# Kernel tuning notes

Hardware: AMD Instinct MI355X
Metric: run time of the kernel (lower is better)

The kernel has to match this reference:

```python
import jax, jax.numpy as jnp
import numpy as np

B, T, C, H = 4, 2048, 1024, 16
D = C // H  # head_dim = 64


def setup_inputs() -> dict:
    key = jax.random.key(0)
    k1, k2, k3, k4 = jax.random.split(key, 4)
    x = jax.random.normal(k1, (B, T, C), dtype=jnp.float32)
    # realistic padding: each sequence has length in [T//2, T]
    lengths = jax.random.randint(k4, (B,), T // 2, T + 1)
    padding_mask = jnp.arange(T)[None, :] < lengths[:, None]  # True = keep
    # weights stored [in, out] (equivalent to torch Linear weight transposed)
    w_qkv = jax.random.normal(k2, (C, 3 * C), dtype=jnp.float32) * (C ** -0.5)
    w_out = jax.random.normal(k3, (C, C), dtype=jnp.float32) * (C ** -0.5)
    b_out = jnp.zeros((C,), dtype=jnp.float32)
    return {"x": x, "padding_mask": padding_mask, "w_qkv": w_qkv, "w_out": w_out, "b_out": b_out}


def reference(x, padding_mask, w_qkv, w_out, b_out):
    scale = D ** -0.5
    qkv = x @ w_qkv  # [B,T,3C]
    q, k, v = jnp.split(qkv, 3, axis=-1)

    def split_heads(t):
        return t.reshape(B, T, H, D).transpose(0, 2, 1, 3)  # [B,H,T,D]

    q, k, v = split_heads(q), split_heads(k), split_heads(v)
    attn = jnp.einsum("bhqd,bhkd->bhqk", q, k) * scale  # [B,H,T,T]
    mask = padding_mask[:, None, None, :]  # [B,1,1,T]
    attn = jnp.where(mask, attn, jnp.finfo(attn.dtype).min)
    attn = jax.nn.softmax(attn, axis=-1)
    # dropout is identity in eval mode
    out = jnp.einsum("bhqk,bhkd->bhqd", attn, v)  # [B,H,T,D]
    out = out.transpose(0, 2, 1, 3).reshape(B, T, C)
    return out @ w_out + b_out
```

## Files before the change

kernel.cpp:

```cpp
#include <hip/hip_runtime.h>
#include <hip/hip_bf16.h>

#define Bb 4
#define Tt 2048
#define Cc 1024
#define Hh 16

typedef unsigned short u16;
typedef __attribute__((ext_vector_type(8))) __bf16 bf16x8;
typedef __attribute__((ext_vector_type(4))) float  f32x4;

__device__ __forceinline__ u16 f2bf_hw(float f) {
    __bf16 h = (__bf16)f;
    return *(u16*)&h;
}

__device__ __forceinline__ unsigned cvt_pk_bf16(float a, float b) {
    unsigned r;
    asm("v_cvt_pk_bf16_f32 %0, %1, %2" : "=v"(r) : "v"(a), "v"(b));
    return r;
}

__device__ __forceinline__ float fexp2(float x) {
#if __has_builtin(__builtin_amdgcn_exp2f)
    return __builtin_amdgcn_exp2f(x);
#else
    return __expf(x * 0.6931471805599453f);
#endif
}

__device__ __forceinline__ void gld_lds16(const void* g, void* l) {
    __builtin_amdgcn_global_load_lds(
        (__attribute__((address_space(1))) void*)(g),
        (__attribute__((address_space(3))) void*)(l),
        16, 0, 0);
}

__device__ __forceinline__ f32x4 mfma16(bf16x8 a, bf16x8 b, f32x4 c) {
    return __builtin_amdgcn_mfma_f32_16x16x32_bf16(a, b, c, 0, 0, 0);
}

__device__ void castT_body(const float* __restrict__ in, u16* __restrict__ out,
                           int K, int N, int scaleN, float sv,
                           int bx, int by, float Ls[64][65]) {
    const int n0 = bx * 64, k0 = by * 64;
    const int t = threadIdx.x;
    #pragma unroll
    for (int s = 0; s < 4; ++s) {
        int idx = t + 256 * s;
        int r   = idx >> 4;
        int c4  = (idx & 15) * 4;
        float4 v = *(const float4*)&in[(size_t)(k0 + r) * N + n0 + c4];
        Ls[r][c4 + 0] = v.x; Ls[r][c4 + 1] = v.y;
        Ls[r][c4 + 2] = v.z; Ls[r][c4 + 3] = v.w;
    }
    __syncthreads();
    #pragma unroll
    for (int s = 0; s < 2; ++s) {
        int idx = t + 256 * s;
        int n   = idx >> 3;
        int kc  = (idx & 7) * 8;
        const float sc = (n0 + n < scaleN) ? sv : 1.0f;
        alignas(16) u16 tmp[8];
        #pragma unroll
        for (int i = 0; i < 8; ++i) tmp[i] = f2bf_hw(Ls[kc + i][n] * sc);
        *(uint4*)&out[(size_t)(n0 + n) * K + k0 + kc] = *(const uint4*)tmp;
    }
}

__global__ void prep_cast(const float* __restrict__ x, u16* __restrict__ xb,
                          const float* __restrict__ w_qkv, u16* __restrict__ wqkvT,
                          const float* __restrict__ w_out, u16* __restrict__ woutT,
                          float c2) {
    __shared__ float Ls[64][65];
    const int id = blockIdx.x;
    if (id < 8192) {
        const int i = id * 256 + threadIdx.x;
        float4 v = ((const float4*)x)[i];
        uint2 o;
        o.x = cvt_pk_bf16(v.x, v.y);
        o.y = cvt_pk_bf16(v.z, v.w);
        ((uint2*)xb)[i] = o;
    } else if (id < 8192 + 768) {
        const int r = id - 8192;
        castT_body(w_qkv, wqkvT, Cc, 3 * Cc, Cc, c2, r % 48, r / 48, Ls);
    } else {
        const int r = id - 8960;
        castT_body(w_out, woutT, Cc, Cc, 0, 1.0f, r % 16, r / 16, Ls);
    }
}

__global__ __launch_bounds__(256, 3) void gemm_bt_bf16(
    const u16* __restrict__ A, const u16* __restrict__ Bt,
    const float* __restrict__ bias,
    u16* __restrict__ outB, float* __restrict__ outF,
    int M, int N, int K)
{
    __shared__ u16 As[128 * 64];
    __shared__ u16 Bs[128 * 64];
    const int t = threadIdx.x;
    const int w = t >> 6, lane = t & 63;
    const int quad = lane >> 4, l16 = lane & 15;
    const int wm = w >> 1, wn = w & 1;
    const int m0 = blockIdx.y * 128, n0 = blockIdx.x * 128;

    const int l8r   = lane >> 3;
    const int g_log = (lane & 7) ^ l8r;
    const u16* sAp[4]; const u16* sBp[4];
    #pragma unroll
    for (int u = 0; u < 4; ++u) {
        const int gi = w * 4 + u;
        sAp[u] = A  + (size_t)(m0 + gi * 8 + l8r) * K + g_log * 8;
        sBp[u] = Bt + (size_t)(n0 + gi * 8 + l8r) * K + g_log * 8;
    }
    const int dst0 = w * 2048 + lane * 8;

    int aoff[4][2], boff[4][2];
    #pragma unroll
    for (int i = 0; i < 4; ++i) {
        const int rA = 64 * wm + 16 * i + l16;
        const int rB = 64 * wn + 16 * i + l16;
        #pragma unroll
        for (int kk = 0; kk < 2; ++kk) {
            aoff[i][kk] = rA * 64 + (((4 * kk + quad) ^ (rA & 7)) * 8);
            boff[i][kk] = rB * 64 + (((4 * kk + quad) ^ (rB & 7)) * 8);
        }
    }

    f32x4 acc[4][4] = {};

    for (int k0 = 0; k0 < K; k0 += 64) {
        __syncthreads();
        #pragma unroll
        for (int u = 0; u < 4; ++u) {
            gld_lds16(sAp[u] + k0, (void*)(As + dst0 + u * 512));
            gld_lds16(sBp[u] + k0, (void*)(Bs + dst0 + u * 512));
        }
        asm volatile("s_waitcnt vmcnt(0)" ::: "memory");
        __syncthreads();

        #pragma unroll
        for (int kk = 0; kk < 2; ++kk) {
            bf16x8 af[4], bfr[4];
            #pragma unroll
            for (int i = 0; i < 4; ++i) af[i]  = *(const bf16x8*)&As[aoff[i][kk]];
            #pragma unroll
            for (int j = 0; j < 4; ++j) bfr[j] = *(const bf16x8*)&Bs[boff[j][kk]];
            #pragma unroll
            for (int i = 0; i < 4; ++i)
                #pragma unroll
                for (int j = 0; j < 4; ++j)
                    acc[i][j] = mfma16(af[i], bfr[j], acc[i][j]);
        }
    }

    const int rbase = m0 + 64 * wm + quad * 4;
    const int cbase = n0 + 64 * wn + l16;
    if (outF) {
        float bv[4];
        #pragma unroll
        for (int j = 0; j < 4; ++j) bv[j] = bias[cbase + 16 * j];
        #pragma unroll
        for (int i = 0; i < 4; ++i)
            #pragma unroll
            for (int r = 0; r < 4; ++r) {
                size_t ro = (size_t)(rbase + 16 * i + r) * N;
                #pragma unroll
                for (int j = 0; j < 4; ++j)
                    outF[ro + cbase + 16 * j] = acc[i][j][r] + bv[j];
            }
    } else {
        #pragma unroll
        for (int i = 0; i < 4; ++i)
            #pragma unroll
            for (int r = 0; r < 4; ++r) {
                size_t ro = (size_t)(rbase + 16 * i + r) * N;
                #pragma unroll
                for (int j = 0; j < 4; ++j)
                    outB[ro + cbase + 16 * j] = f2bf_hw(acc[i][j][r]);
            }
    }
}

__global__ __launch_bounds__(256, 3) void gemm_qkv_bt(
    const u16* __restrict__ A, const u16* __restrict__ Bt,
    u16* __restrict__ outQ, u16* __restrict__ kx, u16* __restrict__ vx)
{
    const int K = Cc;
    __shared__ u16 As[128 * 64];
    __shared__ u16 Bs[128 * 64];
    const int t = threadIdx.x;
    const int w = t >> 6, lane = t & 63;
    const int quad = lane >> 4, l16 = lane & 15;
    const int wm = w >> 1, wn = w & 1;
    const int m0 = blockIdx.y * 128, n0 = blockIdx.x * 128;

    const int l8r   = lane >> 3;
    const int g_log = (lane & 7) ^ l8r;
    const u16* sAp[4]; const u16* sBp[4];
    #pragma unroll
    for (int u = 0; u < 4; ++u) {
        const int gi = w * 4 + u;
        sAp[u] = A  + (size_t)(m0 + gi * 8 + l8r) * K + g_log * 8;
        sBp[u] = Bt + (size_t)(n0 + gi * 8 + l8r) * K + g_log * 8;
    }
    const int dst0 = w * 2048 + lane * 8;

    int aoff[4][2], boff[4][2];
    #pragma unroll
    for (int i = 0; i < 4; ++i) {
        const int rA = 64 * wm + 16 * i + l16;
        const int rB = 64 * wn + 16 * i + l16;
        #pragma unroll
        for (int kk = 0; kk < 2; ++kk) {
            aoff[i][kk] = rA * 64 + (((4 * kk + quad) ^ (rA & 7)) * 8);
            boff[i][kk] = rB * 64 + (((4 * kk + quad) ^ (rB & 7)) * 8);
        }
    }

    f32x4 acc[4][4] = {};

    for (int k0 = 0; k0 < K; k0 += 64) {
        __syncthreads();
        #pragma unroll
        for (int u = 0; u < 4; ++u) {
            gld_lds16(sAp[u] + k0, (void*)(As + dst0 + u * 512));
            gld_lds16(sBp[u] + k0, (void*)(Bs + dst0 + u * 512));
        }
        asm volatile("s_waitcnt vmcnt(0)" ::: "memory");
        __syncthreads();

        #pragma unroll
        for (int kk = 0; kk < 2; ++kk) {
            bf16x8 af[4], bfr[4];
            #pragma unroll
            for (int i = 0; i < 4; ++i) af[i]  = *(const bf16x8*)&As[aoff[i][kk]];
            #pragma unroll
            for (int j = 0; j < 4; ++j) bfr[j] = *(const bf16x8*)&Bs[boff[j][kk]];
            #pragma unroll
            for (int i = 0; i < 4; ++i)
                #pragma unroll
                for (int j = 0; j < 4; ++j)
                    acc[i][j] = mfma16(af[i], bfr[j], acc[i][j]);
        }
    }

    const int rbase = m0 + 64 * wm + quad * 4;
    const int cbase = n0 + 64 * wn + l16;
    const int region = n0 >> 10;

    if (region == 0) {
        #pragma unroll
        for (int i = 0; i < 4; ++i)
            #pragma unroll
            for (int r = 0; r < 4; ++r) {
                size_t ro = (size_t)(rbase + 16 * i + r) * Cc;
                #pragma unroll
                for (int j = 0; j < 4; ++j)
                    outQ[ro + cbase + 16 * j] = f2bf_hw(acc[i][j][r]);
            }
    } else if (region == 1) {
        int colK[4];
        #pragma unroll
        for (int j = 0; j < 4; ++j) {
            const int c = (cbase - 1024) + 16 * j;
            const int h = c >> 6, d = c & 63;
            colK[j] = h * 131072 + (d >> 5) * 512 + ((d >> 3) & 3) * 128 + (d & 7);
        }
        #pragma unroll
        for (int i = 0; i < 4; ++i)
            #pragma unroll
            for (int r = 0; r < 4; ++r) {
                const int row = rbase + 16 * i + r;
                const int b = row >> 11, key = row & 2047;
                const int ch = key >> 6, keyr = key & 63;
                const int rowK = b * 2097152 + ch * 4096 + (keyr >> 4) * 1024 + (keyr & 15) * 8;
                #pragma unroll
                for (int j = 0; j < 4; ++j)
                    kx[rowK + colK[j]] = f2bf_hw(acc[i][j][r]);
            }
    } else {
        int colV[4];
        #pragma unroll
        for (int j = 0; j < 4; ++j) {
            const int c = (cbase - 2048) + 16 * j;
            const int h = c >> 6, d = c & 63;
            colV[j] = h * 131072 + (d >> 4) * 1024 + (d & 15) * 8;
        }
        #pragma unroll
        for (int i = 0; i < 4; ++i)
            #pragma unroll
            for (int r = 0; r < 4; ++r) {
                const int row = rbase + 16 * i + r;
                const int b = row >> 11, key = row & 2047;
                const int ch = key >> 6, keyr = key & 63;
                const int rowV = b * 2097152 + ch * 4096 + (keyr >> 5) * 512
                               + ((keyr >> 3) & 3) * 128 + (keyr & 7);
                #pragma unroll
                for (int j = 0; j < 4; ++j)
                    vx[rowV + colV[j]] = f2bf_hw(acc[i][j][r]);
            }
    }
}

__global__ __launch_bounds__(256, 2) void attn_mfma4(
    const u16* __restrict__ qb, const u16* __restrict__ kx, const u16* __restrict__ vx,
    const int* __restrict__ mask, u16* __restrict__ outO)
{
    __shared__ u16 KVs[8192];
    __shared__ u16 Pss[4][4][16 * 68];

    const int t = threadIdx.x;
    const int w = t >> 6, lane = t & 63;
    const int quad = lane >> 4, l16 = lane & 15;
    const int bh = blockIdx.x, qblk = blockIdx.y, b = bh >> 4, h = bh & 15;

    int sum = 0;
    {
        const int4* mp = (const int4*)(mask + b * Tt) + lane * 8;
        #pragma unroll
        for (int i = 0; i < 8; ++i) { int4 m4 = mp[i]; sum += m4.x + m4.y + m4.z + m4.w; }
        #pragma unroll
        for (int off = 1; off < 64; off <<= 1) sum += __shfl_xor(sum, off);
    }
    const int L = sum;

    const int q0 = qblk * 256 + w * 64;
    bf16x8 qf[4][2];
    #pragma unroll
    for (int qq = 0; qq < 4; ++qq) {
        const u16* qp = qb + (size_t)(b * Tt + q0 + 16 * qq + l16) * Cc + h * 64 + quad * 8;
        qf[qq][0] = *(const bf16x8*)(qp);
        qf[qq][1] = *(const bf16x8*)(qp + 32);
    }

    f32x4 oacc[4][4] = {};
    f32x4 lacc[4]    = {};
    const __bf16 onebf = (__bf16)1.0f;
    const bf16x8 ones  = {onebf, onebf, onebf, onebf, onebf, onebf, onebf, onebf};

    const int nfull = L >> 6;
    const int nch   = (L + 63) >> 6;
    const size_t cb0 = (size_t)bh * 32 * 4096;

    {
        uint4 k0a = *(const uint4*)&kx[cb0 + t * 8];
        uint4 k0b = *(const uint4*)&kx[cb0 + 2048 + t * 8];
        uint4 v0a = *(const uint4*)&vx[cb0 + t * 8];
        uint4 v0b = *(const uint4*)&vx[cb0 + 2048 + t * 8];
        *(uint4*)&KVs[t * 8]        = k0a;
        *(uint4*)&KVs[2048 + t * 8] = k0b;
        *(uint4*)&KVs[4096 + t * 8] = v0a;
        *(uint4*)&KVs[6144 + t * 8] = v0b;
    }
    __syncthreads();

    for (int ch = 0; ch < nch; ++ch) {
        const int cc = (ch + 1 < nch) ? ch + 1 : ch;
        const size_t nb = cb0 + (size_t)cc * 4096;
        uint4 nk0 = *(const uint4*)&kx[nb + t * 8];
        uint4 nk1 = *(const uint4*)&kx[nb + 2048 + t * 8];
        uint4 nv0 = *(const uint4*)&vx[nb + t * 8];
        uint4 nv1 = *(const uint4*)&vx[nb + 2048 + t * 8];

        const u16* Kb = KVs;
        const u16* Vb = KVs + 4096;

        bf16x8 kf[4][2];
        #pragma unroll
        for (int jt = 0; jt < 4; ++jt)
            #pragma unroll
            for (int ks = 0; ks < 2; ++ks)
                kf[jt][ks] = *(const bf16x8*)&Kb[(jt * 2 + ks) * 512 + lane * 8];

        bf16x8 vf[4][2];
        #pragma unroll
        for (int dt = 0; dt < 4; ++dt)
            #pragma unroll
            for (int ks = 0; ks < 2; ++ks)
                vf[dt][ks] = *(const bf16x8*)&Vb[(dt * 2 + ks) * 512 + lane * 8];

        #pragma unroll
        for (int qq = 0; qq < 4; ++qq) {
            u16* Pw = Pss[w][qq];
            f32x4 st[4];
            __builtin_amdgcn_s_setprio(1);
            #pragma unroll
            for (int jt = 0; jt < 4; ++jt) {
                f32x4 z = {0.f, 0.f, 0.f, 0.f};
                z = mfma16(kf[jt][0], qf[qq][0], z);
                st[jt] = mfma16(kf[jt][1], qf[qq][1], z);
            }
            __builtin_amdgcn_s_setprio(0);
            uint2 pk[4];
            if (ch < nfull) {
                #pragma unroll
                for (int jt = 0; jt < 4; ++jt) {
                    pk[jt].x = cvt_pk_bf16(fexp2(st[jt][0]), fexp2(st[jt][1]));
                    pk[jt].y = cvt_pk_bf16(fexp2(st[jt][2]), fexp2(st[jt][3]));
                }
            } else {
                const int kc = ch * 64;
                #pragma unroll
                for (int jt = 0; jt < 4; ++jt) {
                    const int kb = kc + 16 * jt + quad * 4;
                    float e[4];
                    #pragma unroll
                    for (int r = 0; r < 4; ++r)
                        e[r] = (kb + r < L) ? fexp2(st[jt][r]) : 0.f;
                    pk[jt].x = cvt_pk_bf16(e[0], e[1]);
                    pk[jt].y = cvt_pk_bf16(e[2], e[3]);
                }
            }
            #pragma unroll
            for (int jt = 0; jt < 4; ++jt)
                *(uint2*)&Pw[l16 * 68 + 16 * jt + quad * 4] = pk[jt];

            __builtin_amdgcn_s_setprio(1);
            #pragma unroll
            for (int ks = 0; ks < 2; ++ks) {
                const u16* pr = &Pw[l16 * 68 + 32 * ks + quad * 8];
                uint2 pa = *(const uint2*)pr;
                uint2 pb = *(const uint2*)(pr + 4);
                uint4 comb = {pa.x, pa.y, pb.x, pb.y};
                bf16x8 pf = *(const bf16x8*)&comb;
                #pragma unroll
                for (int dt = 0; dt < 4; ++dt)
                    oacc[qq][dt] = mfma16(pf, vf[dt][ks], oacc[qq][dt]);
                lacc[qq] = mfma16(pf, ones, lacc[qq]);
            }
            __builtin_amdgcn_s_setprio(0);
        }

        __syncthreads();
        *(uint4*)&KVs[t * 8]        = nk0;
        *(uint4*)&KVs[2048 + t * 8] = nk1;
        *(uint4*)&KVs[4096 + t * 8] = nv0;
        *(uint4*)&KVs[6144 + t * 8] = nv1;
        __syncthreads();
    }

    #pragma unroll
    for (int qq = 0; qq < 4; ++qq)
        #pragma unroll
        for (int r = 0; r < 4; ++r) {
            const float inv = 1.f / lacc[qq][r];
            const size_t ro = (size_t)(b * Tt + q0 + 16 * qq + quad * 4 + r) * Cc + h * 64 + l16;
            #pragma unroll
            for (int dt = 0; dt < 4; ++dt)
                outO[ro + 16 * dt] = f2bf_hw(oacc[qq][dt][r] * inv);
        }
}

extern "C" void kernel_launch(void* const* d_in, const int* in_sizes, int n_in,
                              void* d_out, int out_size, void* d_ws, size_t ws_size,
                              hipStream_t stream) {
    const float* x     = (const float*)d_in[0];
    const int*   mask  = (const int*)  d_in[1];
    const float* w_qkv = (const float*)d_in[2];
    const float* w_out = (const float*)d_in[3];
    const float* b_out = (const float*)d_in[4];
    float*       outp  = (float*)d_out;

    const int M = Bb * Tt;
    char* ws = (char*)d_ws;
    u16* xb     = (u16*)(ws);
    u16* wqkvT  = (u16*)(ws + (16u << 20));
    u16* woutT  = (u16*)(ws + (22u << 20));
    u16* qbuf   = (u16*)(ws + (24u << 20));
    u16* kx     = (u16*)(ws + (40u << 20));
    u16* vx     = (u16*)(ws + (56u << 20));
    u16* attnO  = (u16*)(ws);

    const float c2 = 0.18033688011112042f;

    prep_cast<<<9216, 256, 0, stream>>>(x, xb, w_qkv, wqkvT, w_out, woutT, c2);

    gemm_qkv_bt<<<dim3(3 * Cc / 128, M / 128), 256, 0, stream>>>(
        xb, wqkvT, qbuf, kx, vx);

    attn_mfma4<<<dim3(Bb * Hh, Tt / 256), 256, 0, stream>>>(qbuf, kx, vx, mask, attnO);

    gemm_bt_bf16<<<dim3(Cc / 128, M / 128), 256, 0, stream>>>(
        attnO, woutT, b_out, nullptr, outp, M, Cc, Cc);
}
```

Baseline: 239.5 us.

## Rewrite attention kernel with 32x32 MFMA, register-resident P, and async LDS double buffering

The attention kernel moves from 16x16x32 to 32x32x16 bf16 MFMA tiles with 8 waves of 32 queries each. The probability tile now stays in registers, rearranged with v_permlane32_swap, which removes the LDS round-trip for P. The row sum is accumulated in scalar registers and combined through LDS, replacing the extra ones-MFMA. K/V chunks are double-buffered with global_load_lds, and the QKV GEMM epilogue rewrites the K/V storage layout to match the new operand order. The risks are lower occupancy (512 threads, one block per CU), K/V fragments now reloaded from LDS for each tile, and a correctness dependence on the new swizzle layouts.

```diff
diff --git a/kernel.cpp b/kernel.cpp
--- a/kernel.cpp
+++ b/kernel.cpp
@@ -9,6 +9,7 @@
 typedef unsigned short u16;
 typedef __attribute__((ext_vector_type(8))) __bf16 bf16x8;
 typedef __attribute__((ext_vector_type(4))) float  f32x4;
+typedef __attribute__((ext_vector_type(16))) float f32x16;
 
 __device__ __forceinline__ u16 f2bf_hw(float f) {
     __bf16 h = (__bf16)f;
@@ -19,6 +20,10 @@
     unsigned r;
     asm("v_cvt_pk_bf16_f32 %0, %1, %2" : "=v"(r) : "v"(a), "v"(b));
     return r;
+}
+
+__device__ __forceinline__ void plswap(unsigned &d, unsigned &s) {
+    asm("v_permlane32_swap_b32 %0, %1" : "+v"(d), "+v"(s));
 }
 
 __device__ __forceinline__ float fexp2(float x) {
@@ -38,6 +43,9 @@
 
 __device__ __forceinline__ f32x4 mfma16(bf16x8 a, bf16x8 b, f32x4 c) {
     return __builtin_amdgcn_mfma_f32_16x16x32_bf16(a, b, c, 0, 0, 0);
+}
+__device__ __forceinline__ f32x16 mfma32(bf16x8 a, bf16x8 b, f32x16 c) {
+    return __builtin_amdgcn_mfma_f32_32x32x16_bf16(a, b, c, 0, 0, 0);
 }
 
 __device__ void castT_body(const float* __restrict__ in, u16* __restrict__ out,
@@ -265,16 +273,17 @@
         for (int j = 0; j < 4; ++j) {
             const int c = (cbase - 1024) + 16 * j;
             const int h = c >> 6, d = c & 63;
-            colK[j] = h * 131072 + (d >> 5) * 512 + ((d >> 3) & 3) * 128 + (d & 7);
+            colK[j] = h * 131072 + (d >> 4) * 512 + ((d >> 3) & 1) * 256 + (d & 7);
         }
         #pragma unroll
         for (int i = 0; i < 4; ++i)
             #pragma unroll
             for (int r = 0; r < 4; ++r) {
                 const int row = rbase + 16 * i + r;
-                const int b = row >> 11, key = row & 2047;
-                const int ch = key >> 6, keyr = key & 63;
-                const int rowK = b * 2097152 + ch * 4096 + (keyr >> 4) * 1024 + (keyr & 15) * 8;
+                const int b = row >> 11, keyb = row & 2047;
+                const int ch = keyb >> 6, keyr = keyb & 63;
+                const int rowK = b * 2097152 + ch * 4096
+                               + (keyr >> 5) * 2048 + (keyr & 31) * 8;
                 #pragma unroll
                 for (int j = 0; j < 4; ++j)
                     kx[rowK + colK[j]] = f2bf_hw(acc[i][j][r]);
@@ -285,17 +294,18 @@
         for (int j = 0; j < 4; ++j) {
             const int c = (cbase - 2048) + 16 * j;
             const int h = c >> 6, d = c & 63;
-            colV[j] = h * 131072 + (d >> 4) * 1024 + (d & 15) * 8;
+            colV[j] = h * 131072 + (d >> 5) * 512 + (d & 31) * 8;
         }
         #pragma unroll
         for (int i = 0; i < 4; ++i)
             #pragma unroll
             for (int r = 0; r < 4; ++r) {
                 const int row = rbase + 16 * i + r;
-                const int b = row >> 11, key = row & 2047;
-                const int ch = key >> 6, keyr = key & 63;
-                const int rowV = b * 2097152 + ch * 4096 + (keyr >> 5) * 512
-                               + ((keyr >> 3) & 3) * 128 + (keyr & 7);
+                const int b = row >> 11, keyb = row & 2047;
+                const int ch = keyb >> 6, keyr = keyb & 63;
+                const int rowV = b * 2097152 + ch * 4096
+                               + (keyr >> 5) * 2048 + ((keyr >> 4) & 1) * 1024
+                               + ((keyr >> 3) & 1) * 256 + (keyr & 7);
                 #pragma unroll
                 for (int j = 0; j < 4; ++j)
                     vx[rowV + colV[j]] = f2bf_hw(acc[i][j][r]);
@@ -303,17 +313,17 @@
     }
 }
 
-__global__ __launch_bounds__(256, 2) void attn_mfma4(
+__global__ __launch_bounds__(512, 1) void attn_mfma32(
     const u16* __restrict__ qb, const u16* __restrict__ kx, const u16* __restrict__ vx,
     const int* __restrict__ mask, u16* __restrict__ outO)
 {
-    __shared__ u16 KVs[8192];
-    __shared__ u16 Pss[4][4][16 * 68];
+    __shared__ u16 KVs[2][8192];
+    __shared__ float LS[8][64];
 
     const int t = threadIdx.x;
     const int w = t >> 6, lane = t & 63;
-    const int quad = lane >> 4, l16 = lane & 15;
-    const int bh = blockIdx.x, qblk = blockIdx.y, b = bh >> 4, h = bh & 15;
+    const int c32 = lane & 31, h5 = lane >> 5;
+    const int bh = blockIdx.x, qblk = blockIdx.y, b = bh >> 4, hh = bh & 15;
 
     int sum = 0;
     {
@@ -325,131 +335,101 @@
     }
     const int L = sum;
 
-    const int q0 = qblk * 256 + w * 64;
-    bf16x8 qf[4][2];
-    #pragma unroll
-    for (int qq = 0; qq < 4; ++qq) {
-        const u16* qp = qb + (size_t)(b * Tt + q0 + 16 * qq + l16) * Cc + h * 64 + quad * 8;
-        qf[qq][0] = *(const bf16x8*)(qp);
-        qf[qq][1] = *(const bf16x8*)(qp + 32);
-    }
-
-    f32x4 oacc[4][4] = {};
-    f32x4 lacc[4]    = {};
-    const __bf16 onebf = (__bf16)1.0f;
-    const bf16x8 ones  = {onebf, onebf, onebf, onebf, onebf, onebf, onebf, onebf};
+    const int q0w = qblk * 256 + w * 32;
+    bf16x8 qf[4];
+    {
+        const u16* qp = qb + (size_t)(b * Tt + q0w + c32) * Cc + hh * 64 + h5 * 8;
+        #pragma unroll
+        for (int ds = 0; ds < 4; ++ds)
+            qf[ds] = *(const bf16x8*)(qp + 16 * ds);
+    }
+
+    f32x16 oacc[2] = {};
+    float ls = 0.f;
 
     const int nfull = L >> 6;
     const int nch   = (L + 63) >> 6;
-    const size_t cb0 = (size_t)bh * 32 * 4096;
-
-    {
-        uint4 k0a = *(const uint4*)&kx[cb0 + t * 8];
-        uint4 k0b = *(const uint4*)&kx[cb0 + 2048 + t * 8];
-        uint4 v0a = *(const uint4*)&vx[cb0 + t * 8];
-        uint4 v0b = *(const uint4*)&vx[cb0 + 2048 + t * 8];
-        *(uint4*)&KVs[t * 8]        = k0a;
-        *(uint4*)&KVs[2048 + t * 8] = k0b;
-        *(uint4*)&KVs[4096 + t * 8] = v0a;
-        *(uint4*)&KVs[6144 + t * 8] = v0b;
-    }
+    const size_t cb0 = (size_t)bh * 131072;
+
+    gld_lds16(kx + cb0 + t * 8, &KVs[0][t * 8]);
+    gld_lds16(vx + cb0 + t * 8, &KVs[0][4096 + t * 8]);
     __syncthreads();
 
     for (int ch = 0; ch < nch; ++ch) {
+        const int p = ch & 1;
         const int cc = (ch + 1 < nch) ? ch + 1 : ch;
         const size_t nb = cb0 + (size_t)cc * 4096;
-        uint4 nk0 = *(const uint4*)&kx[nb + t * 8];
-        uint4 nk1 = *(const uint4*)&kx[nb + 2048 + t * 8];
-        uint4 nv0 = *(const uint4*)&vx[nb + t * 8];
-        uint4 nv1 = *(const uint4*)&vx[nb + 2048 + t * 8];
-
-        const u16* Kb = KVs;
-        const u16* Vb = KVs + 4096;
-
-        bf16x8 kf[4][2];
-        #pragma unroll
-        for (int jt = 0; jt < 4; ++jt)
-            #pragma unroll
-            for (int ks = 0; ks < 2; ++ks)
-                kf[jt][ks] = *(const bf16x8*)&Kb[(jt * 2 + ks) * 512 + lane * 8];
-
-        bf16x8 vf[4][2];
-        #pragma unroll
-        for (int dt = 0; dt < 4; ++dt)
-            #pragma unroll
-            for (int ks = 0; ks < 2; ++ks)
-                vf[dt][ks] = *(const bf16x8*)&Vb[(dt * 2 + ks) * 512 + lane * 8];
-
-        #pragma unroll
-        for (int qq = 0; qq < 4; ++qq) {
-            u16* Pw = Pss[w][qq];
-            f32x4 st[4];
+        gld_lds16(kx + nb + t * 8, &KVs[p ^ 1][t * 8]);
+        gld_lds16(vx + nb + t * 8, &KVs[p ^ 1][4096 + t * 8]);
+
+        const u16* Kb = KVs[p];
+        const u16* Vb = KVs[p] + 4096;
+
+        #pragma unroll
+        for (int jt = 0; jt < 2; ++jt) {
+            f32x16 st = {};
             __builtin_amdgcn_s_setprio(1);
             #pragma unroll
-            for (int jt = 0; jt < 4; ++jt) {
-                f32x4 z = {0.f, 0.f, 0.f, 0.f};
-                z = mfma16(kf[jt][0], qf[qq][0], z);
-                st[jt] = mfma16(kf[jt][1], qf[qq][1], z);
+            for (int ds = 0; ds < 4; ++ds) {
+                bf16x8 kf = *(const bf16x8*)&Kb[jt * 2048 + ds * 512 + lane * 8];
+                st = mfma32(kf, qf[ds], st);
             }
             __builtin_amdgcn_s_setprio(0);
-            uint2 pk[4];
+
+            float e[16];
             if (ch < nfull) {
                 #pragma unroll
-                for (int jt = 0; jt < 4; ++jt) {
-                    pk[jt].x = cvt_pk_bf16(fexp2(st[jt][0]), fexp2(st[jt][1]));
-                    pk[jt].y = cvt_pk_bf16(fexp2(st[jt][2]), fexp2(st[jt][3]));
+                for (int r = 0; r < 16; ++r) e[r] = fexp2(st[r]);
+            } else {
+                const int kcb = ch * 64 + 32 * jt + 4 * h5;
+                #pragma unroll
+                for (int r = 0; r < 16; ++r) {
+                    const int key = kcb + (r & 3) + 8 * (r >> 2);
+                    e[r] = (key < L) ? fexp2(st[r]) : 0.f;
                 }
-            } else {
-                const int kc = ch * 64;
-                #pragma unroll
-                for (int jt = 0; jt < 4; ++jt) {
-                    const int kb = kc + 16 * jt + quad * 4;
-                    float e[4];
-                    #pragma unroll
-                    for (int r = 0; r < 4; ++r)
-                        e[r] = (kb + r < L) ? fexp2(st[jt][r]) : 0.f;
-                    pk[jt].x = cvt_pk_bf16(e[0], e[1]);
-                    pk[jt].y = cvt_pk_bf16(e[2], e[3]);
+            }
+            #pragma unroll
+            for (int r = 0; r < 16; ++r) ls += e[r];
+
+            unsigned W[4][2];
+            #pragma unroll
+            for (int s = 0; s < 4; ++s)
+                #pragma unroll
+                for (int i = 0; i < 2; ++i)
+                    W[s][i] = cvt_pk_bf16(e[4 * s + 2 * i], e[4 * s + 2 * i + 1]);
+
+            #pragma unroll
+            for (int ks = 0; ks < 2; ++ks) {
+                unsigned w0 = W[2 * ks][0], w2 = W[2 * ks + 1][0];
+                unsigned w1 = W[2 * ks][1], w3 = W[2 * ks + 1][1];
+                plswap(w0, w2);
+                plswap(w1, w3);
+                uint4 pfw = {w0, w1, w2, w3};
+                bf16x8 pf = *(const bf16x8*)&pfw;
+                __builtin_amdgcn_s_setprio(1);
+                #pragma unroll
+                for (int dt = 0; dt < 2; ++dt) {
+                    bf16x8 vf = *(const bf16x8*)&Vb[jt * 2048 + ks * 1024 + dt * 512 + lane * 8];
+                    oacc[dt] = mfma32(pf, vf, oacc[dt]);
                 }
-            }
-            #pragma unroll
-            for (int jt = 0; jt < 4; ++jt)
-                *(uint2*)&Pw[l16 * 68 + 16 * jt + quad * 4] = pk[jt];
-
-            __builtin_amdgcn_s_setprio(1);
-            #pragma unroll
-            for (int ks = 0; ks < 2; ++ks) {
-                const u16* pr = &Pw[l16 * 68 + 32 * ks + quad * 8];
-                uint2 pa = *(const uint2*)pr;
-                uint2 pb = *(const uint2*)(pr + 4);
-                uint4 comb = {pa.x, pa.y, pb.x, pb.y};
-                bf16x8 pf = *(const bf16x8*)&comb;
-                #pragma unroll
-                for (int dt = 0; dt < 4; ++dt)
-                    oacc[qq][dt] = mfma16(pf, vf[dt][ks], oacc[qq][dt]);
-                lacc[qq] = mfma16(pf, ones, lacc[qq]);
-            }
-            __builtin_amdgcn_s_setprio(0);
+                __builtin_amdgcn_s_setprio(0);
+            }
         }
 
         __syncthreads();
-        *(uint4*)&KVs[t * 8]        = nk0;
-        *(uint4*)&KVs[2048 + t * 8] = nk1;
-        *(uint4*)&KVs[4096 + t * 8] = nv0;
-        *(uint4*)&KVs[6144 + t * 8] = nv1;
-        __syncthreads();
-    }
-
-    #pragma unroll
-    for (int qq = 0; qq < 4; ++qq)
-        #pragma unroll
-        for (int r = 0; r < 4; ++r) {
-            const float inv = 1.f / lacc[qq][r];
-            const size_t ro = (size_t)(b * Tt + q0 + 16 * qq + quad * 4 + r) * Cc + h * 64 + l16;
-            #pragma unroll
-            for (int dt = 0; dt < 4; ++dt)
-                outO[ro + 16 * dt] = f2bf_hw(oacc[qq][dt][r] * inv);
-        }
+    }
+
+    LS[w][lane] = ls;
+    __syncthreads();
+
+    #pragma unroll
+    for (int r = 0; r < 16; ++r) {
+        const int rowR = (r & 3) + 8 * (r >> 2) + 4 * h5;
+        const float inv = 1.f / (LS[w][rowR] + LS[w][rowR + 32]);
+        const size_t ro = (size_t)(b * Tt + q0w + rowR) * Cc + hh * 64 + c32;
+        outO[ro]      = f2bf_hw(oacc[0][r] * inv);
+        outO[ro + 32] = f2bf_hw(oacc[1][r] * inv);
+    }
 }
 
 extern "C" void kernel_launch(void* const* d_in, const int* in_sizes, int n_in,
@@ -479,7 +459,8 @@
     gemm_qkv_bt<<<dim3(3 * Cc / 128, M / 128), 256, 0, stream>>>(
         xb, wqkvT, qbuf, kx, vx);
 
-    attn_mfma4<<<dim3(Bb * Hh, Tt / 256), 256, 0, stream>>>(qbuf, kx, vx, mask, attnO);
+    attn_mfma32<<<dim3(Bb * Hh, Tt / 256), 512, 0, stream>>>(
+        qbuf, kx, vx, mask, attnO);
 
     gemm_bt_bf16<<<dim3(Cc / 128, M / 128), 256, 0, stream>>>(
         attnO, woutT, b_out, nullptr, outp, M, Cc, Cc);
```

New measurement: 250.8 us. 4.7% more time.
